# Performance work log

Hardware: AMD Instinct MI355X
Metric: run time of the kernel (lower is better)

## Reference

```python
import jax, jax.numpy as jnp
import numpy as np

N = 50000      # nodes
E = 1600000    # directed edges (avg degree 32)
IN, HID, OUT = 512, 256, 128
EPS = 1e-5


def setup_inputs() -> dict:
    key = jax.random.key(0)
    ks = jax.random.split(key, 8)
    x = jax.random.normal(ks[0], (N, IN), dtype=jnp.float32)
    edge_index = jax.random.randint(ks[1], (2, E), 0, N, dtype=jnp.int32)
    # GCNConv weights (glorot-ish scale), bias zeros
    W1 = jax.random.normal(ks[2], (IN, HID), dtype=jnp.float32) * np.sqrt(2.0 / (IN + HID))
    b1 = jnp.zeros((HID,), dtype=jnp.float32)
    W2 = jax.random.normal(ks[3], (HID, OUT), dtype=jnp.float32) * np.sqrt(2.0 / (HID + OUT))
    b2 = jnp.zeros((OUT,), dtype=jnp.float32)
    # PyG LayerNorm affine params (per-channel)
    ln0_w = jnp.ones((IN,), jnp.float32);  ln0_b = jnp.zeros((IN,), jnp.float32)
    ln1_w = jnp.ones((HID,), jnp.float32); ln1_b = jnp.zeros((HID,), jnp.float32)
    ln2_w = jnp.ones((OUT,), jnp.float32); ln2_b = jnp.zeros((OUT,), jnp.float32)
    return {"x": x, "edge_index": edge_index, "W1": W1, "b1": b1, "W2": W2, "b2": b2,
            "ln0_w": ln0_w, "ln0_b": ln0_b, "ln1_w": ln1_w, "ln1_b": ln1_b,
            "ln2_w": ln2_w, "ln2_b": ln2_b}


def layernorm_graph(x, w, b):
    # PyG LayerNorm(mode='graph'): mean/var over all nodes and channels (batch is all-zero)
    mean = jnp.mean(x)
    var = jnp.mean(jnp.square(x - mean))
    return (x - mean) * jax.lax.rsqrt(var + EPS) * w + b


def gcn_conv(x, W, b, src, dst, n):
    # x' = D^-1/2 (A + I) D^-1/2 (x W) + b   (PyG GCNConv with self-loops)
    h = x @ W                                            # [N, F_out]
    loops = jnp.arange(n, dtype=src.dtype)
    src_sl = jnp.concatenate([src, loops])               # [E+N]
    dst_sl = jnp.concatenate([dst, loops])
    deg = jax.ops.segment_sum(jnp.ones(src_sl.shape[0], x.dtype), dst_sl, num_segments=n)
    dinv = jnp.where(deg > 0, jax.lax.rsqrt(deg), 0.0)
    norm = dinv[src_sl] * dinv[dst_sl]                   # [E+N]
    msg = h[src_sl] * norm[:, None]                      # gather + scale
    return jax.ops.segment_sum(msg, dst_sl, num_segments=n) + b


def reference(x, edge_index, W1, b1, W2, b2, ln0_w, ln0_b, ln1_w, ln1_b, ln2_w, ln2_b):
    src, dst = edge_index[0], edge_index[1]
    n = x.shape[0]
    h = layernorm_graph(x, ln0_w, ln0_b)
    h = jax.nn.relu(gcn_conv(h, W1, b1, src, dst, n))
    h = layernorm_graph(h, ln1_w, ln1_b)
    # dropout: inference-mode identity
    h = jax.nn.relu(gcn_conv(h, W2, b2, src, dst, n))
    h = layernorm_graph(h, ln2_w, ln2_b)
    # global_mean_pool with batch == zeros -> mean over all nodes, shape [1, OUT]
    return jnp.mean(h, axis=0, keepdims=True)
```

## Files before the change

kernel.cpp:

```cpp
#include <hip/hip_runtime.h>

typedef unsigned short u16;
typedef __attribute__((ext_vector_type(8))) short bf16x8;
typedef __attribute__((ext_vector_type(4))) float f32x4;

#define IN_F  512
#define HID_F 256
#define OUT_F 128
#define G_STATS 1024

__device__ inline u16 f2bf_rne(float f) {
  unsigned int u = __float_as_uint(f);
  unsigned int r = (u + 0x7fffu + ((u >> 16) & 1u)) >> 16;
  return (u16)r;
}
__device__ inline unsigned int pack_bf2(float lo, float hi) {
  return (unsigned int)f2bf_rne(lo) | ((unsigned int)f2bf_rne(hi) << 16);
}
__device__ inline float bf_lo(unsigned int u) { return __uint_as_float(u << 16); }
__device__ inline float bf_hi(unsigned int u) { return __uint_as_float(u & 0xffff0000u); }

__global__ __launch_bounds__(256) void count_kernel(const int* __restrict__ dst, int E,
                                                    int* __restrict__ counts) {
  int stride = gridDim.x * blockDim.x;
  for (int i = blockIdx.x * blockDim.x + threadIdx.x; i < E; i += stride)
    atomicAdd(&counts[dst[i]], 1);
}

__global__ __launch_bounds__(256) void dinv_kernel(const int* __restrict__ counts,
                                                   float* __restrict__ dinv, int n) {
  int i = blockIdx.x * blockDim.x + threadIdx.x;
  if (i < n) dinv[i] = rsqrtf((float)counts[i] + 1.0f);
}

__global__ __launch_bounds__(1024) void scan_kernel(const int* __restrict__ counts,
                                                    int* __restrict__ row_ptr, int n) {
  __shared__ int wsum[16];
  __shared__ int s_carry, s_total;
  const int tid = threadIdx.x;
  const int lane = tid & 63, wid = tid >> 6;
  if (tid == 0) s_carry = 0;
  __syncthreads();
  const int PER = 8, CH = 1024 * PER;
  for (int base = 0; base < n; base += CH) {
    int i0 = base + tid * PER;
    int v[PER];
    int s = 0;
    if (i0 + PER <= n) {
      int4 a = *(const int4*)&counts[i0];
      int4 b = *(const int4*)&counts[i0 + 4];
      int c[8] = {a.x, a.y, a.z, a.w, b.x, b.y, b.z, b.w};
#pragma unroll
      for (int j = 0; j < 8; ++j) { s += c[j]; v[j] = s; }
    } else {
#pragma unroll
      for (int j = 0; j < PER; ++j) { int i = i0 + j; int c = (i < n) ? counts[i] : 0; s += c; v[j] = s; }
    }
    int ts = s;
#pragma unroll
    for (int off = 1; off < 64; off <<= 1) {
      int o = __shfl_up(ts, off, 64);
      if (lane >= off) ts += o;
    }
    if (lane == 63) wsum[wid] = ts;
    __syncthreads();
    if (tid == 0) {
      int c = 0;
#pragma unroll
      for (int w = 0; w < 16; ++w) { int t = wsum[w]; wsum[w] = c; c += t; }
      s_total = c;
    }
    __syncthreads();
    int base_excl = s_carry + wsum[wid] + (ts - s);
    if (i0 + PER <= n) {
      int4 o0 = make_int4(base_excl, base_excl + v[0], base_excl + v[1], base_excl + v[2]);
      int4 o1 = make_int4(base_excl + v[3], base_excl + v[4], base_excl + v[5], base_excl + v[6]);
      *(int4*)&row_ptr[i0] = o0;
      *(int4*)&row_ptr[i0 + 4] = o1;
    } else {
      for (int j = 0; j < PER; ++j) { int i = i0 + j; if (i < n) row_ptr[i] = base_excl + (j ? v[j - 1] : 0); }
    }
    __syncthreads();
    if (tid == 0) s_carry += s_total;
    __syncthreads();
  }
  if (tid == 0) row_ptr[n] = s_carry;
}

__global__ __launch_bounds__(256) void scatter_kernel(const int* __restrict__ src,
                                                      const int* __restrict__ dst, int E,
                                                      const int* __restrict__ row_ptr,
                                                      int* __restrict__ fill,
                                                      int* __restrict__ csr_src) {
  int stride = gridDim.x * blockDim.x;
  for (int i = blockIdx.x * blockDim.x + threadIdx.x; i < E; i += stride) {
    int d = dst[i];
    int p = row_ptr[d] + atomicAdd(&fill[d], 1);
    csr_src[p] = src[i];
  }
}

__global__ __launch_bounds__(256) void stats_partial(const float4* __restrict__ x, long n4,
                                                     double* __restrict__ psum,
                                                     double* __restrict__ psq) {
  double s = 0.0, q = 0.0;
  long stride = (long)gridDim.x * 256;
  for (long i = (long)blockIdx.x * 256 + threadIdx.x; i < n4; i += stride) {
    float4 v = x[i];
    s += (double)((v.x + v.y) + (v.z + v.w));
    q += (double)v.x * v.x + (double)v.y * v.y + (double)v.z * v.z + (double)v.w * v.w;
  }
  __shared__ double sh[256], sh2[256];
  sh[threadIdx.x] = s; sh2[threadIdx.x] = q;
  __syncthreads();
  for (int off = 128; off > 0; off >>= 1) {
    if (threadIdx.x < off) { sh[threadIdx.x] += sh[threadIdx.x + off]; sh2[threadIdx.x] += sh2[threadIdx.x + off]; }
    __syncthreads();
  }
  if (threadIdx.x == 0) { psum[blockIdx.x] = sh[0]; psq[blockIdx.x] = sh2[0]; }
}

__global__ __launch_bounds__(512) void finalize_ln(const double* __restrict__ psum,
                            const double* __restrict__ psq,
                            int nb, double inv_count,
                            const float* __restrict__ lnw, const float* __restrict__ lnb,
                            float* __restrict__ s, float* __restrict__ t, int C) {
  double a = 0.0, b = 0.0;
  for (int i = threadIdx.x; i < nb; i += blockDim.x) { a += psum[i]; b += psq[i]; }
  __shared__ double sa[512], sb[512];
  sa[threadIdx.x] = a; sb[threadIdx.x] = b;
  __syncthreads();
  for (int off = blockDim.x >> 1; off > 0; off >>= 1) {
    if ((int)threadIdx.x < off) { sa[threadIdx.x] += sa[threadIdx.x + off]; sb[threadIdx.x] += sb[threadIdx.x + off]; }
    __syncthreads();
  }
  double mean = sa[0] * inv_count;
  double var  = sb[0] * inv_count - mean * mean;
  double inv  = 1.0 / sqrt(var + 1e-5);
  int k = threadIdx.x;
  if (k < C) {
    double sc = inv * (double)lnw[k];
    s[k] = (float)sc;
    t[k] = (float)((double)lnb[k] - mean * sc);
  }
}

__global__ __launch_bounds__(256) void wt_kernel(const float* __restrict__ W,
                                                 u16* __restrict__ Wt, int K, int N) {
  __shared__ float tile[32][33];
  int n0 = blockIdx.x * 32, k0 = blockIdx.y * 32;
  int tx = threadIdx.x & 31, ty = threadIdx.x >> 5;
  for (int r = ty; r < 32; r += 8) tile[r][tx] = W[(size_t)(k0 + r) * N + n0 + tx];
  __syncthreads();
  for (int r = ty; r < 32; r += 8) Wt[(size_t)(n0 + r) * K + k0 + tx] = f2bf_rne(tile[tx][r]);
}

__global__ __launch_bounds__(256) void gemm_ln_mfma(const float* __restrict__ X,
                                                    const u16* __restrict__ Bt,
                                                    int M, int K, int N,
                                                    const float* __restrict__ s,
                                                    const float* __restrict__ t,
                                                    const float* __restrict__ dinv,
                                                    u16* __restrict__ H) {
  __shared__ u16 As[128 * 64];
  __shared__ u16 Bs[128 * 64];
  const int tid = threadIdx.x;
  const int lane = tid & 63;
  const int wid = tid >> 6;
  const int wr = wid >> 1, wc = wid & 1;
  const int bm = blockIdx.x * 128;
  const int bn = blockIdx.y * 128;

  f32x4 acc[4][4] = {};

  for (int k0 = 0; k0 < K; k0 += 64) {
#pragma unroll
    for (int i = 0; i < 4; ++i) {
      int g = i * 256 + tid;
      int row = g >> 3;
      int slot = g & 7;
      int gk = k0 + slot * 8;
      int wsi = row * 64 + ((slot ^ (row & 7)) * 8);
      int gm = bm + row;
      uint4 o = make_uint4(0u, 0u, 0u, 0u);
      if (gm < M) {
        float4 v0 = *(const float4*)&X[(size_t)gm * K + gk];
        float4 v1 = *(const float4*)&X[(size_t)gm * K + gk + 4];
        float4 sA = *(const float4*)&s[gk];
        float4 sB = *(const float4*)&s[gk + 4];
        float4 tA = *(const float4*)&t[gk];
        float4 tB = *(const float4*)&t[gk + 4];
        o.x = pack_bf2(fmaf(v0.x, sA.x, tA.x), fmaf(v0.y, sA.y, tA.y));
        o.y = pack_bf2(fmaf(v0.z, sA.z, tA.z), fmaf(v0.w, sA.w, tA.w));
        o.z = pack_bf2(fmaf(v1.x, sB.x, tB.x), fmaf(v1.y, sB.y, tB.y));
        o.w = pack_bf2(fmaf(v1.z, sB.z, tB.z), fmaf(v1.w, sB.w, tB.w));
      }
      *(uint4*)&As[wsi] = o;
      uint4 vb = *(const uint4*)&Bt[(size_t)(bn + row) * K + gk];
      *(uint4*)&Bs[wsi] = vb;
    }
    __syncthreads();
#pragma unroll
    for (int ko = 0; ko < 2; ++ko) {
      bf16x8 af[4], bfr[4];
#pragma unroll
      for (int i = 0; i < 4; ++i) {
        int ar = wr * 64 + i * 16 + (lane & 15);
        int as = (ko * 4 + (lane >> 4)) ^ (ar & 7);
        af[i] = *(const bf16x8*)&As[ar * 64 + as * 8];
        int br = wc * 64 + i * 16 + (lane & 15);
        int bs = (ko * 4 + (lane >> 4)) ^ (br & 7);
        bfr[i] = *(const bf16x8*)&Bs[br * 64 + bs * 8];
      }
#pragma unroll
      for (int mi = 0; mi < 4; ++mi)
#pragma unroll
        for (int ni = 0; ni < 4; ++ni)
          acc[mi][ni] = __builtin_amdgcn_mfma_f32_16x16x32_bf16(af[mi], bfr[ni], acc[mi][ni], 0, 0, 0);
    }
    __syncthreads();
  }

  const int rg = (lane >> 4) * 4;
  const int cn = lane & 15;
#pragma unroll
  for (int mi = 0; mi < 4; ++mi) {
#pragma unroll
    for (int j = 0; j < 4; ++j) {
      int m = bm + wr * 64 + mi * 16 + rg + j;
      if (m < M) {
        float di = dinv[m];
#pragma unroll
        for (int ni = 0; ni < 4; ++ni) {
          int n = bn + wc * 64 + ni * 16 + cn;
          H[(size_t)m * N + n] = f2bf_rne(acc[mi][ni][j] * di);
        }
      }
    }
  }
}

template <int F>
__global__ __launch_bounds__(256) void agg_kernel(const unsigned int* __restrict__ Hs,
                                                  const int* __restrict__ row_ptr,
                                                  const int* __restrict__ csr_src,
                                                  const float* __restrict__ dinv,
                                                  const float* __restrict__ bias,
                                                  float* __restrict__ out, int n,
                                                  double* __restrict__ psum,
                                                  double* __restrict__ psq) {
  constexpr int LPN = F / 2;
  constexpr int NODES = 256 / LPN;
  int node = blockIdx.x * NODES + threadIdx.x / LPN;
  int f2 = threadIdx.x % LPN;
  float r0 = 0.f, r1 = 0.f;
  if (node < n) {
    unsigned int su = Hs[(size_t)node * LPN + f2];
    float a0 = bf_lo(su), a1 = bf_hi(su);
    float b0 = 0.f, b1 = 0.f, c0 = 0.f, c1 = 0.f, d0 = 0.f, d1 = 0.f;
    int e = row_ptr[node];
    const int e1 = row_ptr[node + 1];
    for (; e + 4 <= e1; e += 4) {
      int s0 = csr_src[e], s1 = csr_src[e + 1], s2 = csr_src[e + 2], s3 = csr_src[e + 3];
      unsigned int u0 = Hs[(size_t)s0 * LPN + f2];
      unsigned int u1 = Hs[(size_t)s1 * LPN + f2];
      unsigned int u2 = Hs[(size_t)s2 * LPN + f2];
      unsigned int u3 = Hs[(size_t)s3 * LPN + f2];
      a0 += bf_lo(u0); a1 += bf_hi(u0);
      b0 += bf_lo(u1); b1 += bf_hi(u1);
      c0 += bf_lo(u2); c1 += bf_hi(u2);
      d0 += bf_lo(u3); d1 += bf_hi(u3);
    }
    for (; e < e1; ++e) {
      int s0 = csr_src[e];
      unsigned int u0 = Hs[(size_t)s0 * LPN + f2];
      a0 += bf_lo(u0); a1 += bf_hi(u0);
    }
    float di = dinv[node];
    float2 bv = *(const float2*)&bias[2 * f2];
    r0 = fmaxf(fmaf(di, (a0 + b0) + (c0 + d0), bv.x), 0.f);
    r1 = fmaxf(fmaf(di, (a1 + b1) + (c1 + d1), bv.y), 0.f);
    float2 o = make_float2(r0, r1);
    *(float2*)&out[(size_t)node * F + 2 * f2] = o;
  }
  __shared__ double sh[256], sh2[256];
  sh[threadIdx.x] = (double)r0 + (double)r1;
  sh2[threadIdx.x] = (double)r0 * r0 + (double)r1 * r1;
  __syncthreads();
  for (int off = 128; off > 0; off >>= 1) {
    if ((int)threadIdx.x < off) { sh[threadIdx.x] += sh[threadIdx.x + off]; sh2[threadIdx.x] += sh2[threadIdx.x + off]; }
    __syncthreads();
  }
  if (threadIdx.x == 0) { psum[blockIdx.x] = sh[0]; psq[blockIdx.x] = sh2[0]; }
}

#define AGG2_NITER 8
__global__ __launch_bounds__(256) void agg_colstats(const unsigned int* __restrict__ Hs,
                                                    const int* __restrict__ row_ptr,
                                                    const int* __restrict__ csr_src,
                                                    const float* __restrict__ dinv,
                                                    const float* __restrict__ bias,
                                                    int n,
                                                    double* __restrict__ colpart,
                                                    double* __restrict__ qpart) {
  constexpr int F = OUT_F;
  constexpr int LPN = F / 2;
  constexpr int NODES = 256 / LPN;
  const int f2 = threadIdx.x % LPN;
  const int grp = threadIdx.x / LPN;
  float2 bv = *(const float2*)&bias[2 * f2];
  double cs0 = 0.0, cs1 = 0.0, q = 0.0;
  for (int it = 0; it < AGG2_NITER; ++it) {
    int node = (blockIdx.x * AGG2_NITER + it) * NODES + grp;
    if (node < n) {
      unsigned int su = Hs[(size_t)node * LPN + f2];
      float a0 = bf_lo(su), a1 = bf_hi(su);
      float b0 = 0.f, b1 = 0.f, c0 = 0.f, c1 = 0.f, d0 = 0.f, d1 = 0.f;
      int e = row_ptr[node];
      const int e1 = row_ptr[node + 1];
      for (; e + 4 <= e1; e += 4) {
        int s0 = csr_src[e], s1 = csr_src[e + 1], s2 = csr_src[e + 2], s3 = csr_src[e + 3];
        unsigned int u0 = Hs[(size_t)s0 * LPN + f2];
        unsigned int u1 = Hs[(size_t)s1 * LPN + f2];
        unsigned int u2 = Hs[(size_t)s2 * LPN + f2];
        unsigned int u3 = Hs[(size_t)s3 * LPN + f2];
        a0 += bf_lo(u0); a1 += bf_hi(u0);
        b0 += bf_lo(u1); b1 += bf_hi(u1);
        c0 += bf_lo(u2); c1 += bf_hi(u2);
        d0 += bf_lo(u3); d1 += bf_hi(u3);
      }
      for (; e < e1; ++e) {
        int s0 = csr_src[e];
        unsigned int u0 = Hs[(size_t)s0 * LPN + f2];
        a0 += bf_lo(u0); a1 += bf_hi(u0);
      }
      float di = dinv[node];
      float r0 = fmaxf(fmaf(di, (a0 + b0) + (c0 + d0), bv.x), 0.f);
      float r1 = fmaxf(fmaf(di, (a1 + b1) + (c1 + d1), bv.y), 0.f);
      cs0 += (double)r0; cs1 += (double)r1;
      q += (double)r0 * r0 + (double)r1 * r1;
    }
  }
  __shared__ double sh0[256], sh1[256], shq[256];
  sh0[threadIdx.x] = cs0; sh1[threadIdx.x] = cs1; shq[threadIdx.x] = q;
  __syncthreads();
  if (grp == 0) {
#pragma unroll
    for (int g = 1; g < NODES; ++g) {
      sh0[threadIdx.x] += sh0[threadIdx.x + g * LPN];
      sh1[threadIdx.x] += sh1[threadIdx.x + g * LPN];
    }
    colpart[(size_t)blockIdx.x * F + 2 * f2]     = sh0[threadIdx.x];
    colpart[(size_t)blockIdx.x * F + 2 * f2 + 1] = sh1[threadIdx.x];
  }
  for (int off = 128; off > 0; off >>= 1) {
    if ((int)threadIdx.x < off) shq[threadIdx.x] += shq[threadIdx.x + off];
    __syncthreads();
  }
  if (threadIdx.x == 0) qpart[blockIdx.x] = shq[0];
}

__global__ __launch_bounds__(1024) void final_kernel(const double* __restrict__ colpart,
                                                     const double* __restrict__ qpart, int B, int n,
                                                     const float* __restrict__ lnw,
                                                     const float* __restrict__ lnb,
                                                     float* __restrict__ out) {
  __shared__ double shc[1024], shq[1024];
  const int tid = threadIdx.x;
  const int col = tid & 127, slice = tid >> 7;
  double s = 0.0;
  for (int b = slice; b < B; b += 8) s += colpart[(size_t)b * OUT_F + col];
  double q = 0.0;
  for (int b = tid; b < B; b += 1024) q += qpart[b];
  shc[tid] = s; shq[tid] = q;
  __syncthreads();
  for (int off = 512; off > 0; off >>= 1) {
    if (tid < off) shq[tid] += shq[tid + off];
    __syncthreads();
  }
  double cs = 0.0;
  if (tid < 128) {
#pragma unroll
    for (int sl = 0; sl < 8; ++sl) cs += shc[sl * 128 + col];
  }
  double qtot = shq[0];
  __syncthreads();
  shc[tid] = (tid < 128) ? cs : 0.0;
  __syncthreads();
  for (int off = 64; off > 0; off >>= 1) {
    if (tid < off) shc[tid] += shc[tid + off];
    __syncthreads();
  }
  if (tid < 128) {
    double cnt = (double)n * (double)OUT_F;
    double mean = shc[0] / cnt;
    double var = qtot / cnt - mean * mean;
    double inv = 1.0 / sqrt(var + 1e-5);
    double colmean = cs / (double)n;
    out[tid] = (float)((colmean - mean) * inv * (double)lnw[tid] + (double)lnb[tid]);
  }
}

extern "C" void kernel_launch(void* const* d_in, const int* in_sizes, int n_in,
                              void* d_out, int out_size, void* d_ws, size_t ws_size,
                              hipStream_t stream) {
  const float* x   = (const float*)d_in[0];
  const int*  ei   = (const int*)d_in[1];
  const float* W1  = (const float*)d_in[2];
  const float* b1  = (const float*)d_in[3];
  const float* W2  = (const float*)d_in[4];
  const float* b2  = (const float*)d_in[5];
  const float* ln0w = (const float*)d_in[6];
  const float* ln0b = (const float*)d_in[7];
  const float* ln1w = (const float*)d_in[8];
  const float* ln1b = (const float*)d_in[9];
  const float* ln2w = (const float*)d_in[10];
  const float* ln2b = (const float*)d_in[11];

  const int N = in_sizes[0] / IN_F;
  const int E = in_sizes[1] / 2;
  const int Mpad = ((N + 127) / 128) * 128;
  const int* src = ei;
  const int* dst = ei + E;

  const int agg1_blocks = (N + 1) / 2;
  const int agg2_blocks = (N + 4 * AGG2_NITER - 1) / (4 * AGG2_NITER);

  char* ws = (char*)d_ws;
  size_t off = 0;
  auto alloc = [&](size_t bytes) -> void* {
    void* p = ws + off;
    off += (bytes + 255) & ~(size_t)255;
    return p;
  };
  int*    counts  = (int*)alloc((size_t)N * 4);
  int*    fill    = (int*)alloc((size_t)N * 4);
  size_t zero_bytes = off;
  float*  dinv    = (float*)alloc((size_t)N * 4);
  int*    row_ptr = (int*)alloc((size_t)(N + 8) * 4);
  int*    csr_src = (int*)alloc((size_t)E * 4);
  int     nb_max  = agg1_blocks > G_STATS ? agg1_blocks : G_STATS;
  double* psum    = (double*)alloc((size_t)nb_max * 8);
  double* psq     = (double*)alloc((size_t)nb_max * 8);
  double* colpart = (double*)alloc((size_t)agg2_blocks * OUT_F * 8);
  double* qpart   = (double*)alloc((size_t)agg2_blocks * 8);
  float*  s0      = (float*)alloc(IN_F * 4);
  float*  t0      = (float*)alloc(IN_F * 4);
  float*  s1      = (float*)alloc(HID_F * 4);
  float*  t1      = (float*)alloc(HID_F * 4);
  u16*    Wt1     = (u16*)alloc((size_t)HID_F * IN_F * 2);
  u16*    Wt2     = (u16*)alloc((size_t)OUT_F * HID_F * 2);
  u16*    h1      = (u16*)alloc((size_t)N * HID_F * 2);
  float*  c1      = (float*)alloc((size_t)N * HID_F * 4);
  u16*    h2 = h1;

  hipMemsetAsync(ws, 0, zero_bytes, stream);

  count_kernel<<<1024, 256, 0, stream>>>(dst, E, counts);
  dinv_kernel<<<(N + 255) / 256, 256, 0, stream>>>(counts, dinv, N);
  scan_kernel<<<1, 1024, 0, stream>>>(counts, row_ptr, N);
  scatter_kernel<<<1024, 256, 0, stream>>>(src, dst, E, row_ptr, fill, csr_src);

  wt_kernel<<<dim3(HID_F / 32, IN_F / 32), 256, 0, stream>>>(W1, Wt1, IN_F, HID_F);
  wt_kernel<<<dim3(OUT_F / 32, HID_F / 32), 256, 0, stream>>>(W2, Wt2, HID_F, OUT_F);

  stats_partial<<<G_STATS, 256, 0, stream>>>((const float4*)x, (long)N * IN_F / 4, psum, psq);
  finalize_ln<<<1, 512, 0, stream>>>(psum, psq, G_STATS, 1.0 / ((double)N * IN_F), ln0w, ln0b, s0, t0, IN_F);

  gemm_ln_mfma<<<dim3(Mpad / 128, HID_F / 128), 256, 0, stream>>>(x, Wt1, N, IN_F, HID_F, s0, t0, dinv, h1);
  agg_kernel<HID_F><<<agg1_blocks, 256, 0, stream>>>((const unsigned int*)h1, row_ptr, csr_src,
                                                     dinv, b1, c1, N, psum, psq);
  finalize_ln<<<1, 512, 0, stream>>>(psum, psq, agg1_blocks, 1.0 / ((double)N * HID_F), ln1w, ln1b, s1, t1, HID_F);

  gemm_ln_mfma<<<dim3(Mpad / 128, OUT_F / 128), 256, 0, stream>>>(c1, Wt2, N, HID_F, OUT_F, s1, t1, dinv, h2);
  agg_colstats<<<agg2_blocks, 256, 0, stream>>>((const unsigned int*)h2, row_ptr, csr_src,
                                                dinv, b2, N, colpart, qpart);

  final_kernel<<<1, 1024, 0, stream>>>(colpart, qpart, agg2_blocks, N, ln2w, ln2b, (float*)d_out);
}
```

Before: 701.5 us.

## Parallelize final column reduction across blocks and shrink agg2 per-block work

Templates the MFMA GEMM on warp columns so the B-tile width can vary, though both launches still use WN=2, so that part behaves as before. Cuts AGG2_NITER from 8 to 2, which gives the second aggregation four times as many blocks for better GPU occupancy. This also makes the per-block partial arrays larger. To keep the final reduction cheap, the single-block final kernel is replaced by a 129-block column-reduction kernel plus a tiny finalize kernel, at the cost of one extra launch.

```diff
diff --git a/kernel.cpp b/kernel.cpp
--- a/kernel.cpp
+++ b/kernel.cpp
@@ -155,28 +155,32 @@
   for (int r = ty; r < 32; r += 8) Wt[(size_t)(n0 + r) * K + k0 + tx] = f2bf_rne(tile[tx][r]);
 }
 
-__global__ __launch_bounds__(256) void gemm_ln_mfma(const float* __restrict__ X,
-                                                    const u16* __restrict__ Bt,
-                                                    int M, int K, int N,
-                                                    const float* __restrict__ s,
-                                                    const float* __restrict__ t,
-                                                    const float* __restrict__ dinv,
-                                                    u16* __restrict__ H) {
+template <int WN>
+__global__ __launch_bounds__(128 * WN) void gemm_ln_mfma(const float* __restrict__ X,
+                                                         const u16* __restrict__ Bt,
+                                                         int M, int K, int N,
+                                                         const float* __restrict__ s,
+                                                         const float* __restrict__ t,
+                                                         const float* __restrict__ dinv,
+                                                         u16* __restrict__ H) {
+  constexpr int BN = WN * 64;
+  constexpr int THREADS = 128 * WN;
   __shared__ u16 As[128 * 64];
-  __shared__ u16 Bs[128 * 64];
+  __shared__ u16 Bs[BN * 64];
   const int tid = threadIdx.x;
   const int lane = tid & 63;
   const int wid = tid >> 6;
-  const int wr = wid >> 1, wc = wid & 1;
+  const int wr = wid / WN;
+  const int wc = wid % WN;
   const int bm = blockIdx.x * 128;
-  const int bn = blockIdx.y * 128;
+  const int bn = blockIdx.y * BN;
 
   f32x4 acc[4][4] = {};
 
   for (int k0 = 0; k0 < K; k0 += 64) {
 #pragma unroll
-    for (int i = 0; i < 4; ++i) {
-      int g = i * 256 + tid;
+    for (int i = 0; i < 1024 / THREADS; ++i) {
+      int g = i * THREADS + tid;
       int row = g >> 3;
       int slot = g & 7;
       int gk = k0 + slot * 8;
@@ -196,7 +200,14 @@
         o.w = pack_bf2(fmaf(v1.z, sB.z, tB.z), fmaf(v1.w, sB.w, tB.w));
       }
       *(uint4*)&As[wsi] = o;
-      uint4 vb = *(const uint4*)&Bt[(size_t)(bn + row) * K + gk];
+    }
+#pragma unroll
+    for (int i = 0; i < (BN * 8) / THREADS; ++i) {
+      int g = i * THREADS + tid;
+      int row = g >> 3;
+      int slot = g & 7;
+      int wsi = row * 64 + ((slot ^ (row & 7)) * 8);
+      uint4 vb = *(const uint4*)&Bt[(size_t)(bn + row) * K + k0 + slot * 8];
       *(uint4*)&Bs[wsi] = vb;
     }
     __syncthreads();
@@ -294,7 +305,7 @@
   if (threadIdx.x == 0) { psum[blockIdx.x] = sh[0]; psq[blockIdx.x] = sh2[0]; }
 }
 
-#define AGG2_NITER 8
+#define AGG2_NITER 2
 __global__ __launch_bounds__(256) void agg_colstats(const unsigned int* __restrict__ Hs,
                                                     const int* __restrict__ row_ptr,
                                                     const int* __restrict__ csr_src,
@@ -360,45 +371,45 @@
   if (threadIdx.x == 0) qpart[blockIdx.x] = shq[0];
 }
 
-__global__ __launch_bounds__(1024) void final_kernel(const double* __restrict__ colpart,
-                                                     const double* __restrict__ qpart, int B, int n,
-                                                     const float* __restrict__ lnw,
-                                                     const float* __restrict__ lnb,
-                                                     float* __restrict__ out) {
-  __shared__ double shc[1024], shq[1024];
-  const int tid = threadIdx.x;
-  const int col = tid & 127, slice = tid >> 7;
+__global__ __launch_bounds__(256) void colred_kernel(const double* __restrict__ colpart,
+                                                     const double* __restrict__ qpart, int B,
+                                                     double* __restrict__ colsum) {
+  const int b = blockIdx.x;
   double s = 0.0;
-  for (int b = slice; b < B; b += 8) s += colpart[(size_t)b * OUT_F + col];
-  double q = 0.0;
-  for (int b = tid; b < B; b += 1024) q += qpart[b];
-  shc[tid] = s; shq[tid] = q;
-  __syncthreads();
-  for (int off = 512; off > 0; off >>= 1) {
-    if (tid < off) shq[tid] += shq[tid + off];
-    __syncthreads();
-  }
-  double cs = 0.0;
-  if (tid < 128) {
-#pragma unroll
-    for (int sl = 0; sl < 8; ++sl) cs += shc[sl * 128 + col];
-  }
-  double qtot = shq[0];
-  __syncthreads();
-  shc[tid] = (tid < 128) ? cs : 0.0;
+  if (b < OUT_F) {
+    for (int i = threadIdx.x; i < B; i += 256) s += colpart[(size_t)i * OUT_F + b];
+  } else {
+    for (int i = threadIdx.x; i < B; i += 256) s += qpart[i];
+  }
+  __shared__ double sh[256];
+  sh[threadIdx.x] = s;
+  __syncthreads();
+  for (int off = 128; off > 0; off >>= 1) {
+    if ((int)threadIdx.x < off) sh[threadIdx.x] += sh[threadIdx.x + off];
+    __syncthreads();
+  }
+  if (threadIdx.x == 0) colsum[b] = sh[0];
+}
+
+__global__ __launch_bounds__(128) void final_kernel(const double* __restrict__ colsum, int n,
+                                                    const float* __restrict__ lnw,
+                                                    const float* __restrict__ lnb,
+                                                    float* __restrict__ out) {
+  const int c = threadIdx.x;
+  double cs = colsum[c];
+  __shared__ double sh[128];
+  sh[c] = cs;
   __syncthreads();
   for (int off = 64; off > 0; off >>= 1) {
-    if (tid < off) shc[tid] += shc[tid + off];
-    __syncthreads();
-  }
-  if (tid < 128) {
-    double cnt = (double)n * (double)OUT_F;
-    double mean = shc[0] / cnt;
-    double var = qtot / cnt - mean * mean;
-    double inv = 1.0 / sqrt(var + 1e-5);
-    double colmean = cs / (double)n;
-    out[tid] = (float)((colmean - mean) * inv * (double)lnw[tid] + (double)lnb[tid]);
-  }
+    if (c < off) sh[c] += sh[c + off];
+    __syncthreads();
+  }
+  double cnt = (double)n * (double)OUT_F;
+  double mean = sh[0] / cnt;
+  double var = colsum[OUT_F] / cnt - mean * mean;
+  double inv = 1.0 / sqrt(var + 1e-5);
+  double colmean = cs / (double)n;
+  out[c] = (float)((colmean - mean) * inv * (double)lnw[c] + (double)lnb[c]);
 }
 
 extern "C" void kernel_launch(void* const* d_in, const int* in_sizes, int n_in,
@@ -444,6 +455,7 @@
   double* psq     = (double*)alloc((size_t)nb_max * 8);
   double* colpart = (double*)alloc((size_t)agg2_blocks * OUT_F * 8);
   double* qpart   = (double*)alloc((size_t)agg2_blocks * 8);
+  double* colsum  = (double*)alloc((size_t)(OUT_F + 1) * 8);
   float*  s0      = (float*)alloc(IN_F * 4);
   float*  t0      = (float*)alloc(IN_F * 4);
   float*  s1      = (float*)alloc(HID_F * 4);
@@ -467,14 +479,15 @@
   stats_partial<<<G_STATS, 256, 0, stream>>>((const float4*)x, (long)N * IN_F / 4, psum, psq);
   finalize_ln<<<1, 512, 0, stream>>>(psum, psq, G_STATS, 1.0 / ((double)N * IN_F), ln0w, ln0b, s0, t0, IN_F);
 
-  gemm_ln_mfma<<<dim3(Mpad / 128, HID_F / 128), 256, 0, stream>>>(x, Wt1, N, IN_F, HID_F, s0, t0, dinv, h1);
+  gemm_ln_mfma<2><<<dim3(Mpad / 128, HID_F / 128), 256, 0, stream>>>(x, Wt1, N, IN_F, HID_F, s0, t0, dinv, h1);
   agg_kernel<HID_F><<<agg1_blocks, 256, 0, stream>>>((const unsigned int*)h1, row_ptr, csr_src,
                                                      dinv, b1, c1, N, psum, psq);
   finalize_ln<<<1, 512, 0, stream>>>(psum, psq, agg1_blocks, 1.0 / ((double)N * HID_F), ln1w, ln1b, s1, t1, HID_F);
 
-  gemm_ln_mfma<<<dim3(Mpad / 128, OUT_F / 128), 256, 0, stream>>>(c1, Wt2, N, HID_F, OUT_F, s1, t1, dinv, h2);
+  gemm_ln_mfma<2><<<dim3(Mpad / 128, OUT_F / 128), 256, 0, stream>>>(c1, Wt2, N, HID_F, OUT_F, s1, t1, dinv, h2);
   agg_colstats<<<agg2_blocks, 256, 0, stream>>>((const unsigned int*)h2, row_ptr, csr_src,
                                                 dinv, b2, N, colpart, qpart);
 
-  final_kernel<<<1, 1024, 0, stream>>>(colpart, qpart, agg2_blocks, N, ln2w, ln2b, (float*)d_out);
-}
+  colred_kernel<<<OUT_F + 1, 256, 0, stream>>>(colpart, qpart, agg2_blocks, colsum);
+  final_kernel<<<1, 128, 0, stream>>>(colsum, N, ln2w, ln2b, (float*)d_out);
+}
```

Result: faster. 650.7 us (-7.2%).
